# Kernel optimization log

Measured on AMD Instinct MI355X. Metric: run time of the kernel, lower is better.

Reference implementation:

```python
import jax, jax.numpy as jnp
import numpy as np

N, E = 100000, 1000000
IN_F, HID, OUT, K = 64, 64, 32, 3


def setup_inputs() -> dict:
    key = jax.random.key(0)
    ks = jax.random.split(key, 8)
    s = 0.05
    return {
        "features": jax.random.normal(ks[0], (N, IN_F), dtype=jnp.float32),
        "src": jax.random.randint(ks[1], (E,), 0, N),
        "dst": jax.random.randint(ks[2], (E,), 0, N),
        "n_nodes": N,
        "W1": jax.random.normal(ks[3], (K * IN_F, HID), jnp.float32) * s,
        "b1": jnp.zeros((HID,), jnp.float32),
        "W2": jax.random.normal(ks[4], (K * HID, HID), jnp.float32) * s,
        "b2": jnp.zeros((HID,), jnp.float32),
        "Wm1": jax.random.normal(ks[5], (HID, HID), jnp.float32) * s,
        "bm1": jnp.zeros((HID,), jnp.float32),
        "Wm2": jax.random.normal(ks[6], (HID, OUT), jnp.float32) * s,
        "bm2": jnp.zeros((OUT,), jnp.float32),
    }


def _cheb_conv(x, src, dst, dinv, W, b, n_nodes, k=K):
    # DGL ChebConv with lambda_max = 2 (re_norm = 2/lambda_max = 1).
    def prop(h):  # D^{-1/2} A D^{-1/2} h via edge gather/scatter
        m = (h * dinv)[src]                                   # [E, F]
        agg = jax.ops.segment_sum(m, dst, num_segments=n_nodes)
        return agg * dinv

    X0 = x
    Xs = [X0]
    X1 = -prop(X0)                 # -re_norm*L h + (re_norm-1)*X0, re_norm=1
    Xs.append(X1)
    for _ in range(2, k):
        Xi = -2.0 * prop(X1) - X0  # Chebyshev recursion
        Xs.append(Xi)
        X0, X1 = X1, Xi
    return jnp.concatenate(Xs, axis=1) @ W + b  # Linear(k*F_in -> F_out)


def reference(features, src, dst, n_nodes, W1, b1, W2, b2, Wm1, bm1, Wm2, bm2):
    deg = jax.ops.segment_sum(
        jnp.ones((src.shape[0],), dtype=features.dtype), dst, num_segments=n_nodes
    )
    dinv = (jnp.clip(deg, 1.0, None) ** -0.5)[:, None]  # in-degree^{-1/2}
    x = jax.nn.relu(_cheb_conv(features, src, dst, dinv, W1, b1, n_nodes))
    x = jax.nn.relu(_cheb_conv(x, src, dst, dinv, W2, b2, n_nodes))
    return jax.nn.relu(x @ Wm1 + bm1) @ Wm2 + bm2
```

## Files before the change

### kernel.cpp

```cpp
#include <hip/hip_runtime.h>


typedef unsigned short ushort_t;

__device__ inline ushort_t f2bf(float f) {
    unsigned u = __float_as_uint(f);
    return (ushort_t)((u + 0x7FFFu + ((u >> 16) & 1u)) >> 16);
}
__device__ inline float bf2f(ushort_t h) {
    return __uint_as_float(((unsigned)h) << 16);
}

#define BSH 9
#define BSZ (1 << BSH)
#define CHUNK 4096

__global__ __launch_bounds__(256) void k_bhist(const int* __restrict__ dst,
                                               int* __restrict__ gbase, int E, int NB) {
    __shared__ int h[1024];
    for (int i = threadIdx.x; i < NB; i += 256) h[i] = 0;
    __syncthreads();
    for (int i = blockIdx.x * blockDim.x + threadIdx.x; i < E; i += gridDim.x * blockDim.x)
        atomicAdd(&h[dst[i] >> BSH], 1);
    __syncthreads();
    for (int i = threadIdx.x; i < NB; i += 256)
        if (h[i]) atomicAdd(&gbase[i], h[i]);
}

__global__ void k_bscan(int* __restrict__ gbase, int* __restrict__ gcur, int NB) {
    __shared__ int sh[1024];
    int t = threadIdx.x;
    int v = (t < NB) ? gbase[t] : 0;
    sh[t] = v;
    __syncthreads();
    for (int off = 1; off < 1024; off <<= 1) {
        int u = 0;
        if (t >= off) u = sh[t - off];
        __syncthreads();
        sh[t] += u;
        __syncthreads();
    }
    if (t < NB) {
        int excl = sh[t] - v;
        gbase[t] = excl;
        gcur[t] = excl;
    }
}

__global__ __launch_bounds__(256) void k_bucket2(
    const int* __restrict__ src, const int* __restrict__ dst,
    int* __restrict__ gcur, int2* __restrict__ eb, int E, int NB) {
    __shared__ int ls[CHUNK];
    __shared__ int ld[CHUNK];
    __shared__ int hist[1024];
    __shared__ int bbase[1024];
    int t = threadIdx.x;
    int base = blockIdx.x * CHUNK;
    int count = E - base;
    if (count > CHUNK) count = CHUNK;
    for (int i = t; i < NB; i += 256) hist[i] = 0;
    __syncthreads();
    for (int i = t; i < count; i += 256) {
        int s = src[base + i];
        int d = dst[base + i];
        ls[i] = s;
        ld[i] = d;
        atomicAdd(&hist[d >> BSH], 1);
    }
    __syncthreads();
    for (int b = t; b < NB; b += 256) {
        int c = hist[b];
        bbase[b] = c ? atomicAdd(&gcur[b], c) : 0;
        hist[b] = 0;
    }
    __syncthreads();
    for (int i = t; i < count; i += 256) {
        int d = ld[i];
        int b = d >> BSH;
        int off = atomicAdd(&hist[b], 1);
        eb[bbase[b] + off] = make_int2(ls[i], d);
    }
}

__global__ __launch_bounds__(256) void k_local(
    const int2* __restrict__ eb, const int* __restrict__ gbase,
    int* __restrict__ col, int* __restrict__ row_ptr,
    float* __restrict__ dinv, int N, int E, int NB) {
    __shared__ int cnt[BSZ];
    __shared__ int tsum[256];
    int t = threadIdx.x;
    int b = blockIdx.x;
    int d0 = b << BSH;
    cnt[2 * t] = 0;
    cnt[2 * t + 1] = 0;
    __syncthreads();
    int beg = gbase[b];
    int end = (b + 1 < NB) ? gbase[b + 1] : E;
    for (int i = beg + t; i < end; i += 256)
        atomicAdd(&cnt[eb[i].y - d0], 1);
    __syncthreads();
    int c0 = cnt[2 * t], c1 = cnt[2 * t + 1];
    int mysum = c0 + c1;
    tsum[t] = mysum;
    __syncthreads();
    for (int off = 1; off < 256; off <<= 1) {
        int u = 0;
        if (t >= off) u = tsum[t - off];
        __syncthreads();
        tsum[t] += u;
        __syncthreads();
    }
    int rbase = beg + tsum[t] - mysum;
    int d = d0 + 2 * t;
    if (d < N) {
        row_ptr[d] = rbase;
        dinv[d] = rsqrtf(fmaxf((float)c0, 1.0f));
    }
    if (d + 1 < N) {
        row_ptr[d + 1] = rbase + c0;
        dinv[d + 1] = rsqrtf(fmaxf((float)c1, 1.0f));
    }
    cnt[2 * t] = rbase;
    cnt[2 * t + 1] = rbase + c0;
    __syncthreads();
    for (int i = beg + t; i < end; i += 256) {
        int2 e = eb[i];
        int p = atomicAdd(&cnt[e.y - d0], 1);
        col[p] = e.x;
    }
    if (b == NB - 1 && t == 0) row_ptr[N] = E;
}

__global__ void k_tobf16(const float4* __restrict__ X, const float* __restrict__ dinv,
                         ushort4* __restrict__ Y, int n4) {
    int i = blockIdx.x * blockDim.x + threadIdx.x;
    if (i < n4) {
        float s = dinv[i >> 4];
        float4 v = X[i];
        ushort4 o;
        o.x = f2bf(v.x * s); o.y = f2bf(v.y * s); o.z = f2bf(v.z * s); o.w = f2bf(v.w * s);
        Y[i] = o;
    }
}

template <int MODE>
__global__ __launch_bounds__(256) void k_prop(
    const ushort_t* __restrict__ Xb, const int* __restrict__ rp,
    const int* __restrict__ col, const float* __restrict__ dinv,
    const ushort_t* __restrict__ X0b, ushort_t* __restrict__ OUTB, int N) {
    int wid = (blockIdx.x * blockDim.x + threadIdx.x) >> 6;
    int lane = threadIdx.x & 63;
    if (wid >= N) return;
    int g = lane >> 4;
    int fl = (lane & 15) * 4;
    int beg = rp[wid], end = rp[wid + 1];
    float4 a0 = make_float4(0.f, 0.f, 0.f, 0.f);
    float4 a1 = make_float4(0.f, 0.f, 0.f, 0.f);
    int e = beg + g;
    for (; e + 4 < end; e += 8) {
        int s0 = col[e], s1 = col[e + 4];
        ushort4 u0 = *(const ushort4*)&Xb[(size_t)s0 * 64 + fl];
        ushort4 u1 = *(const ushort4*)&Xb[(size_t)s1 * 64 + fl];
        a0.x += bf2f(u0.x); a0.y += bf2f(u0.y); a0.z += bf2f(u0.z); a0.w += bf2f(u0.w);
        a1.x += bf2f(u1.x); a1.y += bf2f(u1.y); a1.z += bf2f(u1.z); a1.w += bf2f(u1.w);
    }
    if (e < end) {
        int s0 = col[e];
        ushort4 u0 = *(const ushort4*)&Xb[(size_t)s0 * 64 + fl];
        a0.x += bf2f(u0.x); a0.y += bf2f(u0.y); a0.z += bf2f(u0.z); a0.w += bf2f(u0.w);
    }
    float4 acc;
    acc.x = a0.x + a1.x;
    acc.y = a0.y + a1.y;
    acc.z = a0.z + a1.z;
    acc.w = a0.w + a1.w;
    acc.x += __shfl_xor(acc.x, 16);
    acc.y += __shfl_xor(acc.y, 16);
    acc.z += __shfl_xor(acc.z, 16);
    acc.w += __shfl_xor(acc.w, 16);
    acc.x += __shfl_xor(acc.x, 32);
    acc.y += __shfl_xor(acc.y, 32);
    acc.z += __shfl_xor(acc.z, 32);
    acc.w += __shfl_xor(acc.w, 32);
    if (g == 0) {
        float di = dinv[wid];
        float4 o;
        if (MODE == 1) {
            float m = -di * di;
            o.x = m * acc.x; o.y = m * acc.y; o.z = m * acc.z; o.w = m * acc.w;
        } else {
            ushort4 x0u = *(const ushort4*)&X0b[(size_t)wid * 64 + fl];
            float m = -2.0f * di;
            float rd = 1.0f / di;
            o.x = fmaf(m, acc.x, -rd * bf2f(x0u.x));
            o.y = fmaf(m, acc.y, -rd * bf2f(x0u.y));
            o.z = fmaf(m, acc.z, -rd * bf2f(x0u.z));
            o.w = fmaf(m, acc.w, -rd * bf2f(x0u.w));
        }
        ushort4 ob;
        ob.x = f2bf(o.x); ob.y = f2bf(o.y); ob.z = f2bf(o.z); ob.w = f2bf(o.w);
        *(ushort4*)&OUTB[(size_t)wid * 64 + fl] = ob;
    }
}

template <bool SCALE_OUT>
__global__ __launch_bounds__(256) void k_cheb_gemm(
    const ushort_t* __restrict__ X0, const ushort_t* __restrict__ X1,
    const ushort_t* __restrict__ X2, const float* __restrict__ dinv,
    const float* __restrict__ W, const float* __restrict__ b,
    ushort_t* __restrict__ Yb, int N) {
    __shared__ float Ws[64][64];
    __shared__ float Xs[64][68];
    __shared__ float bs[64];
    int t = threadIdx.x;
    if (t < 64) bs[t] = b[t];

    int c4 = (t & 15) * 4;
    int r4 = (t >> 4) * 4;
    int node0 = blockIdx.x * 64;
    float acc[4][4] = {{0}};

    const ushort_t* Xp[3] = {X0, X1, X2};
#pragma unroll 1
    for (int chunk = 0; chunk < 3; chunk++) {
        __syncthreads();
        {
            const float* Wc = W + chunk * 64 * 64;
            for (int i = t; i < 64 * 16; i += 256) {
                int r = i >> 4, c = (i & 15) * 4;
                *(float4*)&Ws[r][c] = *(const float4*)&Wc[r * 64 + c];
            }
        }
        {
            const ushort_t* X = Xp[chunk];
            bool unscale = (chunk < 2);
            int f4 = (t & 15) * 4;
            int nl0 = t >> 4;
            for (int p = 0; p < 4; p++) {
                int nl = nl0 + p * 16;
                int node = node0 + nl;
                float4 v = make_float4(0.f, 0.f, 0.f, 0.f);
                if (node < N) {
                    ushort4 u = *(const ushort4*)&X[(size_t)node * 64 + f4];
                    float r = unscale ? (1.0f / dinv[node]) : 1.0f;
                    v = make_float4(r * bf2f(u.x), r * bf2f(u.y),
                                    r * bf2f(u.z), r * bf2f(u.w));
                }
                *(float4*)&Xs[nl][f4] = v;
            }
        }
        __syncthreads();
#pragma unroll 4
        for (int k4 = 0; k4 < 64; k4 += 4) {
            float4 xv[4], wv[4];
#pragma unroll
            for (int i = 0; i < 4; i++) xv[i] = *(const float4*)&Xs[r4 + i][k4];
#pragma unroll
            for (int q = 0; q < 4; q++) wv[q] = *(const float4*)&Ws[k4 + q][c4];
#pragma unroll
            for (int i = 0; i < 4; i++) {
                acc[i][0] = fmaf(xv[i].x, wv[0].x, acc[i][0]);
                acc[i][1] = fmaf(xv[i].x, wv[0].y, acc[i][1]);
                acc[i][2] = fmaf(xv[i].x, wv[0].z, acc[i][2]);
                acc[i][3] = fmaf(xv[i].x, wv[0].w, acc[i][3]);
                acc[i][0] = fmaf(xv[i].y, wv[1].x, acc[i][0]);
                acc[i][1] = fmaf(xv[i].y, wv[1].y, acc[i][1]);
                acc[i][2] = fmaf(xv[i].y, wv[1].z, acc[i][2]);
                acc[i][3] = fmaf(xv[i].y, wv[1].w, acc[i][3]);
                acc[i][0] = fmaf(xv[i].z, wv[2].x, acc[i][0]);
                acc[i][1] = fmaf(xv[i].z, wv[2].y, acc[i][1]);
                acc[i][2] = fmaf(xv[i].z, wv[2].z, acc[i][2]);
                acc[i][3] = fmaf(xv[i].z, wv[2].w, acc[i][3]);
                acc[i][0] = fmaf(xv[i].w, wv[3].x, acc[i][0]);
                acc[i][1] = fmaf(xv[i].w, wv[3].y, acc[i][1]);
                acc[i][2] = fmaf(xv[i].w, wv[3].z, acc[i][2]);
                acc[i][3] = fmaf(xv[i].w, wv[3].w, acc[i][3]);
            }
        }
    }
#pragma unroll
    for (int i = 0; i < 4; i++) {
        int row = node0 + r4 + i;
        if (row < N) {
            float s = SCALE_OUT ? dinv[row] : 1.0f;
            ushort4 ob;
            ob.x = f2bf(s * fmaxf(acc[i][0] + bs[c4 + 0], 0.0f));
            ob.y = f2bf(s * fmaxf(acc[i][1] + bs[c4 + 1], 0.0f));
            ob.z = f2bf(s * fmaxf(acc[i][2] + bs[c4 + 2], 0.0f));
            ob.w = f2bf(s * fmaxf(acc[i][3] + bs[c4 + 3], 0.0f));
            *(ushort4*)&Yb[(size_t)row * 64 + c4] = ob;
        }
    }
}

__global__ __launch_bounds__(256) void k_mlp_gemm(
    const ushort_t* __restrict__ Hb, const float* __restrict__ Wm1,
    const float* __restrict__ bm1, const float* __restrict__ Wm2,
    const float* __restrict__ bm2, float* __restrict__ out, int N) {
    __shared__ float W1s[64][64];
    __shared__ float W2s[64][32];
    __shared__ float Hs[64][68];
    __shared__ float b1s[64];
    __shared__ float b2s[32];
    int t = threadIdx.x;
    for (int i = t; i < 64 * 16; i += 256) {
        int r = i >> 4, c = (i & 15) * 4;
        *(float4*)&W1s[r][c] = *(const float4*)&Wm1[r * 64 + c];
    }
    for (int i = t; i < 64 * 8; i += 256) {
        int r = i >> 3, c = (i & 7) * 4;
        *(float4*)&W2s[r][c] = *(const float4*)&Wm2[r * 32 + c];
    }
    if (t < 64) b1s[t] = bm1[t];
    else if (t < 96) b2s[t - 64] = bm2[t - 64];

    int node0 = blockIdx.x * 64;
    {
        int f4 = (t & 15) * 4;
        int nl0 = t >> 4;
        for (int p = 0; p < 4; p++) {
            int nl = nl0 + p * 16;
            int node = node0 + nl;
            float4 v = make_float4(0.f, 0.f, 0.f, 0.f);
            if (node < N) {
                ushort4 u = *(const ushort4*)&Hb[(size_t)node * 64 + f4];
                v = make_float4(bf2f(u.x), bf2f(u.y), bf2f(u.z), bf2f(u.w));
            }
            *(float4*)&Hs[nl][f4] = v;
        }
    }
    __syncthreads();

    float acc[4][4] = {{0}};
    int c4 = (t & 15) * 4;
    int r4 = (t >> 4) * 4;
#pragma unroll 4
    for (int k4 = 0; k4 < 64; k4 += 4) {
        float4 xv[4], wv[4];
#pragma unroll
        for (int i = 0; i < 4; i++) xv[i] = *(const float4*)&Hs[r4 + i][k4];
#pragma unroll
        for (int q = 0; q < 4; q++) wv[q] = *(const float4*)&W1s[k4 + q][c4];
#pragma unroll
        for (int i = 0; i < 4; i++) {
            acc[i][0] = fmaf(xv[i].x, wv[0].x, acc[i][0]);
            acc[i][1] = fmaf(xv[i].x, wv[0].y, acc[i][1]);
            acc[i][2] = fmaf(xv[i].x, wv[0].z, acc[i][2]);
            acc[i][3] = fmaf(xv[i].x, wv[0].w, acc[i][3]);
            acc[i][0] = fmaf(xv[i].y, wv[1].x, acc[i][0]);
            acc[i][1] = fmaf(xv[i].y, wv[1].y, acc[i][1]);
            acc[i][2] = fmaf(xv[i].y, wv[1].z, acc[i][2]);
            acc[i][3] = fmaf(xv[i].y, wv[1].w, acc[i][3]);
            acc[i][0] = fmaf(xv[i].z, wv[2].x, acc[i][0]);
            acc[i][1] = fmaf(xv[i].z, wv[2].y, acc[i][1]);
            acc[i][2] = fmaf(xv[i].z, wv[2].z, acc[i][2]);
            acc[i][3] = fmaf(xv[i].z, wv[2].w, acc[i][3]);
            acc[i][0] = fmaf(xv[i].w, wv[3].x, acc[i][0]);
            acc[i][1] = fmaf(xv[i].w, wv[3].y, acc[i][1]);
            acc[i][2] = fmaf(xv[i].w, wv[3].z, acc[i][2]);
            acc[i][3] = fmaf(xv[i].w, wv[3].w, acc[i][3]);
        }
    }
    __syncthreads();
#pragma unroll
    for (int i = 0; i < 4; i++) {
        float4 o;
        o.x = fmaxf(acc[i][0] + b1s[c4 + 0], 0.0f);
        o.y = fmaxf(acc[i][1] + b1s[c4 + 1], 0.0f);
        o.z = fmaxf(acc[i][2] + b1s[c4 + 2], 0.0f);
        o.w = fmaxf(acc[i][3] + b1s[c4 + 3], 0.0f);
        *(float4*)&Hs[r4 + i][c4] = o;
    }
    __syncthreads();

    {
        int cc4 = (t & 7) * 4;
        int r2 = (t >> 3) * 2;
        float a2[2][4] = {{0}};
#pragma unroll 4
        for (int k4 = 0; k4 < 64; k4 += 4) {
            float4 xv[2], wv[4];
#pragma unroll
            for (int i = 0; i < 2; i++) xv[i] = *(const float4*)&Hs[r2 + i][k4];
#pragma unroll
            for (int q = 0; q < 4; q++) wv[q] = *(const float4*)&W2s[k4 + q][cc4];
#pragma unroll
            for (int i = 0; i < 2; i++) {
                a2[i][0] = fmaf(xv[i].x, wv[0].x, a2[i][0]);
                a2[i][1] = fmaf(xv[i].x, wv[0].y, a2[i][1]);
                a2[i][2] = fmaf(xv[i].x, wv[0].z, a2[i][2]);
                a2[i][3] = fmaf(xv[i].x, wv[0].w, a2[i][3]);
                a2[i][0] = fmaf(xv[i].y, wv[1].x, a2[i][0]);
                a2[i][1] = fmaf(xv[i].y, wv[1].y, a2[i][1]);
                a2[i][2] = fmaf(xv[i].y, wv[1].z, a2[i][2]);
                a2[i][3] = fmaf(xv[i].y, wv[1].w, a2[i][3]);
                a2[i][0] = fmaf(xv[i].z, wv[2].x, a2[i][0]);
                a2[i][1] = fmaf(xv[i].z, wv[2].y, a2[i][1]);
                a2[i][2] = fmaf(xv[i].z, wv[2].z, a2[i][2]);
                a2[i][3] = fmaf(xv[i].z, wv[2].w, a2[i][3]);
                a2[i][0] = fmaf(xv[i].w, wv[3].x, a2[i][0]);
                a2[i][1] = fmaf(xv[i].w, wv[3].y, a2[i][1]);
                a2[i][2] = fmaf(xv[i].w, wv[3].z, a2[i][2]);
                a2[i][3] = fmaf(xv[i].w, wv[3].w, a2[i][3]);
            }
        }
#pragma unroll
        for (int i = 0; i < 2; i++) {
            int row = node0 + r2 + i;
            if (row < N) {
                float4 o;
                o.x = a2[i][0] + b2s[cc4 + 0];
                o.y = a2[i][1] + b2s[cc4 + 1];
                o.z = a2[i][2] + b2s[cc4 + 2];
                o.w = a2[i][3] + b2s[cc4 + 3];
                *(float4*)&out[(size_t)row * 32 + cc4] = o;
            }
        }
    }
}

extern "C" void kernel_launch(void* const* d_in, const int* in_sizes, int n_in,
                              void* d_out, int out_size, void* d_ws, size_t ws_size,
                              hipStream_t stream) {
    const float* features = (const float*)d_in[0];
    const int* src = (const int*)d_in[1];
    const int* dst = (const int*)d_in[2];
    const float* W1 = (const float*)d_in[4];
    const float* b1 = (const float*)d_in[5];
    const float* W2 = (const float*)d_in[6];
    const float* b2 = (const float*)d_in[7];
    const float* Wm1 = (const float*)d_in[8];
    const float* bm1 = (const float*)d_in[9];
    const float* Wm2 = (const float*)d_in[10];
    const float* bm2 = (const float*)d_in[11];
    float* out = (float*)d_out;

    int N = in_sizes[0] / 64;
    int E = in_sizes[1];
    int NB = (N + BSZ - 1) >> BSH;

    float* ws = (float*)d_ws;
    float* dinv = ws;
    int* row_ptr = (int*)(dinv + N);
    int* gbase = row_ptr + (N + 1);
    int* gcur = gbase + 1024;
    int* col = gcur + 1024;
    int2* eb = (int2*)(((uintptr_t)(col + E) + 7) & ~(uintptr_t)7);
    ushort_t* Fb  = (ushort_t*)(eb + E);
    ushort_t* X1b = Fb  + (size_t)N * 64;
    ushort_t* X2b = X1b + (size_t)N * 64;
    ushort_t* H1b = X2b + (size_t)N * 64;
    ushort_t* H2b = H1b + (size_t)N * 64;

    int pblk = (N * 64 + 255) / 256;
    int gblk = (N + 63) / 64;
    int n4 = N * 16;
    int cblk = (n4 + 255) / 256;
    int bblk = (E + CHUNK - 1) / CHUNK;

    hipMemsetAsync(gbase, 0, NB * sizeof(int), stream);
    k_bhist<<<512, 256, 0, stream>>>(dst, gbase, E, NB);
    k_bscan<<<1, 1024, 0, stream>>>(gbase, gcur, NB);
    k_bucket2<<<bblk, 256, 0, stream>>>(src, dst, gcur, eb, E, NB);
    k_local<<<NB, 256, 0, stream>>>(eb, gbase, col, row_ptr, dinv, N, E, NB);

    k_tobf16<<<cblk, 256, 0, stream>>>((const float4*)features, dinv, (ushort4*)Fb, n4);

    k_prop<1><<<pblk, 256, 0, stream>>>(Fb, row_ptr, col, dinv, nullptr, X1b, N);
    k_prop<2><<<pblk, 256, 0, stream>>>(X1b, row_ptr, col, dinv, Fb, X2b, N);
    k_cheb_gemm<true><<<gblk, 256, 0, stream>>>(Fb, X1b, X2b, dinv, W1, b1, H1b, N);

    k_prop<1><<<pblk, 256, 0, stream>>>(H1b, row_ptr, col, dinv, nullptr, X1b, N);
    k_prop<2><<<pblk, 256, 0, stream>>>(X1b, row_ptr, col, dinv, H1b, X2b, N);
    k_cheb_gemm<false><<<gblk, 256, 0, stream>>>(H1b, X1b, X2b, dinv, W2, b2, H2b, N);

    k_mlp_gemm<<<gblk, 256, 0, stream>>>(H2b, Wm1, bm1, Wm2, bm2, out, N);
}
```

Baseline: 429.1 us.

## Replace FP32 SIMT GEMMs with bf16 MFMA for Chebyshev and MLP layers

Rewrites the Chebyshev linear layers and the final MLP to use 16x16x32 bf16 MFMA instructions. A new prep kernel converts the weights to transposed bf16. The Chebyshev GEMM keeps separate accumulators for the dinv-scaled and unscaled chunks, so the per-row rescale moves from the operand load into the epilogue. This removes the shared-memory staging and FP32 FMA loops, but quantises the weights to bf16 and writes outputs with narrower, scalar stores.

```diff
diff --git a/kernel.cpp b/kernel.cpp
--- a/kernel.cpp
+++ b/kernel.cpp
@@ -2,6 +2,8 @@
 
 
 typedef unsigned short ushort_t;
+typedef __attribute__((ext_vector_type(8))) short v8s;
+typedef __attribute__((ext_vector_type(4))) float v4f;
 
 __device__ inline ushort_t f2bf(float f) {
     unsigned u = __float_as_uint(f);
@@ -14,6 +16,7 @@
 #define BSH 9
 #define BSZ (1 << BSH)
 #define CHUNK 4096
+
 
 __global__ __launch_bounds__(256) void k_bhist(const int* __restrict__ dst,
                                                int* __restrict__ gbase, int E, int NB) {
@@ -129,6 +132,20 @@
         col[p] = e.x;
     }
     if (b == NB - 1 && t == 0) row_ptr[N] = E;
+}
+
+__global__ void k_wprep(const float* __restrict__ W1, const float* __restrict__ W2,
+                        const float* __restrict__ Wm1, const float* __restrict__ Wm2,
+                        ushort_t* __restrict__ W1t, ushort_t* __restrict__ W2t,
+                        ushort_t* __restrict__ Wm1t, ushort_t* __restrict__ Wm2t) {
+    int i = blockIdx.x * 256 + threadIdx.x;
+    if (i < 12288) { int k = i >> 6, n = i & 63; W1t[n * 192 + k] = f2bf(W1[i]); return; }
+    i -= 12288;
+    if (i < 12288) { int k = i >> 6, n = i & 63; W2t[n * 192 + k] = f2bf(W2[i]); return; }
+    i -= 12288;
+    if (i < 4096) { int k = i >> 6, n = i & 63; Wm1t[n * 64 + k] = f2bf(Wm1[i]); return; }
+    i -= 4096;
+    if (i < 2048) { int k = i >> 5, n = i & 31; Wm2t[n * 64 + k] = f2bf(Wm2[i]); }
 }
 
 __global__ void k_tobf16(const float4* __restrict__ X, const float* __restrict__ dinv,
@@ -204,217 +221,111 @@
 }
 
 template <bool SCALE_OUT>
-__global__ __launch_bounds__(256) void k_cheb_gemm(
+__global__ __launch_bounds__(256) void k_cheb_mfma(
     const ushort_t* __restrict__ X0, const ushort_t* __restrict__ X1,
     const ushort_t* __restrict__ X2, const float* __restrict__ dinv,
-    const float* __restrict__ W, const float* __restrict__ b,
-    ushort_t* __restrict__ Yb, int N) {
-    __shared__ float Ws[64][64];
-    __shared__ float Xs[64][68];
-    __shared__ float bs[64];
-    int t = threadIdx.x;
-    if (t < 64) bs[t] = b[t];
-
-    int c4 = (t & 15) * 4;
-    int r4 = (t >> 4) * 4;
+    const ushort_t* __restrict__ Wt,
+    const float* __restrict__ b, ushort_t* __restrict__ Yb, int N) {
+    int wave = threadIdx.x >> 6, lane = threadIdx.x & 63;
+    int n16 = lane & 15, q = lane >> 4;
     int node0 = blockIdx.x * 64;
-    float acc[4][4] = {{0}};
-
-    const ushort_t* Xp[3] = {X0, X1, X2};
-#pragma unroll 1
-    for (int chunk = 0; chunk < 3; chunk++) {
-        __syncthreads();
-        {
-            const float* Wc = W + chunk * 64 * 64;
-            for (int i = t; i < 64 * 16; i += 256) {
-                int r = i >> 4, c = (i & 15) * 4;
-                *(float4*)&Ws[r][c] = *(const float4*)&Wc[r * 64 + c];
+    int arow = node0 + wave * 16 + n16;
+    const ushort_t* Xc[3] = {X0, X1, X2};
+
+    v4f acc_s[4], acc_u[4];
+#pragma unroll
+    for (int t = 0; t < 4; t++) {
+        acc_s[t] = (v4f){0.f, 0.f, 0.f, 0.f};
+        acc_u[t] = (v4f){0.f, 0.f, 0.f, 0.f};
+    }
+
+#pragma unroll
+    for (int ks = 0; ks < 6; ks++) {
+        int c = ks >> 1;
+        int kk = (ks & 1) * 32 + q * 8;
+        v8s av = {0, 0, 0, 0, 0, 0, 0, 0};
+        if (arow < N) av = *(const v8s*)&Xc[c][(size_t)arow * 64 + kk];
+#pragma unroll
+        for (int t = 0; t < 4; t++) {
+            v8s bv = *(const v8s*)&Wt[(size_t)(t * 16 + n16) * 192 + ks * 32 + q * 8];
+            if (c < 2)
+                acc_s[t] = __builtin_amdgcn_mfma_f32_16x16x32_bf16(av, bv, acc_s[t], 0, 0, 0);
+            else
+                acc_u[t] = __builtin_amdgcn_mfma_f32_16x16x32_bf16(av, bv, acc_u[t], 0, 0, 0);
+        }
+    }
+
+    int rbase = node0 + wave * 16 + q * 4;
+#pragma unroll
+    for (int r = 0; r < 4; r++) {
+        int row = rbase + r;
+        if (row < N) {
+            float dv = dinv[row];
+            float rd = 1.0f / dv;
+            float s = SCALE_OUT ? dv : 1.0f;
+#pragma unroll
+            for (int t = 0; t < 4; t++) {
+                float y = fmaf(rd, acc_s[t][r], acc_u[t][r]) + b[t * 16 + n16];
+                y = fmaxf(y, 0.0f);
+                Yb[(size_t)row * 64 + t * 16 + n16] = f2bf(s * y);
             }
         }
-        {
-            const ushort_t* X = Xp[chunk];
-            bool unscale = (chunk < 2);
-            int f4 = (t & 15) * 4;
-            int nl0 = t >> 4;
-            for (int p = 0; p < 4; p++) {
-                int nl = nl0 + p * 16;
-                int node = node0 + nl;
-                float4 v = make_float4(0.f, 0.f, 0.f, 0.f);
-                if (node < N) {
-                    ushort4 u = *(const ushort4*)&X[(size_t)node * 64 + f4];
-                    float r = unscale ? (1.0f / dinv[node]) : 1.0f;
-                    v = make_float4(r * bf2f(u.x), r * bf2f(u.y),
-                                    r * bf2f(u.z), r * bf2f(u.w));
-                }
-                *(float4*)&Xs[nl][f4] = v;
-            }
-        }
-        __syncthreads();
-#pragma unroll 4
-        for (int k4 = 0; k4 < 64; k4 += 4) {
-            float4 xv[4], wv[4];
-#pragma unroll
-            for (int i = 0; i < 4; i++) xv[i] = *(const float4*)&Xs[r4 + i][k4];
-#pragma unroll
-            for (int q = 0; q < 4; q++) wv[q] = *(const float4*)&Ws[k4 + q][c4];
-#pragma unroll
-            for (int i = 0; i < 4; i++) {
-                acc[i][0] = fmaf(xv[i].x, wv[0].x, acc[i][0]);
-                acc[i][1] = fmaf(xv[i].x, wv[0].y, acc[i][1]);
-                acc[i][2] = fmaf(xv[i].x, wv[0].z, acc[i][2]);
-                acc[i][3] = fmaf(xv[i].x, wv[0].w, acc[i][3]);
-                acc[i][0] = fmaf(xv[i].y, wv[1].x, acc[i][0]);
-                acc[i][1] = fmaf(xv[i].y, wv[1].y, acc[i][1]);
-                acc[i][2] = fmaf(xv[i].y, wv[1].z, acc[i][2]);
-                acc[i][3] = fmaf(xv[i].y, wv[1].w, acc[i][3]);
-                acc[i][0] = fmaf(xv[i].z, wv[2].x, acc[i][0]);
-                acc[i][1] = fmaf(xv[i].z, wv[2].y, acc[i][1]);
-                acc[i][2] = fmaf(xv[i].z, wv[2].z, acc[i][2]);
-                acc[i][3] = fmaf(xv[i].z, wv[2].w, acc[i][3]);
-                acc[i][0] = fmaf(xv[i].w, wv[3].x, acc[i][0]);
-                acc[i][1] = fmaf(xv[i].w, wv[3].y, acc[i][1]);
-                acc[i][2] = fmaf(xv[i].w, wv[3].z, acc[i][2]);
-                acc[i][3] = fmaf(xv[i].w, wv[3].w, acc[i][3]);
-            }
-        }
-    }
-#pragma unroll
-    for (int i = 0; i < 4; i++) {
-        int row = node0 + r4 + i;
+    }
+}
+
+__global__ __launch_bounds__(256) void k_mlp_mfma(
+    const ushort_t* __restrict__ Hb, const ushort_t* __restrict__ W1t,
+    const float* __restrict__ b1, const ushort_t* __restrict__ W2t,
+    const float* __restrict__ b2, float* __restrict__ out, int N) {
+    __shared__ ushort_t Hs[64][76];
+    int wave = threadIdx.x >> 6, lane = threadIdx.x & 63;
+    int n16 = lane & 15, q = lane >> 4;
+    int node0 = blockIdx.x * 64;
+    int arow = node0 + wave * 16 + n16;
+
+    v4f acc[4];
+#pragma unroll
+    for (int t = 0; t < 4; t++) acc[t] = (v4f){0.f, 0.f, 0.f, 0.f};
+#pragma unroll
+    for (int ks = 0; ks < 2; ks++) {
+        v8s av = {0, 0, 0, 0, 0, 0, 0, 0};
+        if (arow < N) av = *(const v8s*)&Hb[(size_t)arow * 64 + ks * 32 + q * 8];
+#pragma unroll
+        for (int t = 0; t < 4; t++) {
+            v8s bv = *(const v8s*)&W1t[(size_t)(t * 16 + n16) * 64 + ks * 32 + q * 8];
+            acc[t] = __builtin_amdgcn_mfma_f32_16x16x32_bf16(av, bv, acc[t], 0, 0, 0);
+        }
+    }
+    int lr = wave * 16 + q * 4;
+#pragma unroll
+    for (int r = 0; r < 4; r++)
+#pragma unroll
+        for (int t = 0; t < 4; t++) {
+            float y = acc[t][r] + b1[t * 16 + n16];
+            Hs[lr + r][t * 16 + n16] = f2bf(fmaxf(y, 0.0f));
+        }
+    __syncthreads();
+
+    v4f a2[2];
+    a2[0] = (v4f){0.f, 0.f, 0.f, 0.f};
+    a2[1] = (v4f){0.f, 0.f, 0.f, 0.f};
+#pragma unroll
+    for (int ks = 0; ks < 2; ks++) {
+        v8s av = *(const v8s*)&Hs[wave * 16 + n16][ks * 32 + q * 8];
+#pragma unroll
+        for (int t = 0; t < 2; t++) {
+            v8s bv = *(const v8s*)&W2t[(size_t)(t * 16 + n16) * 64 + ks * 32 + q * 8];
+            a2[t] = __builtin_amdgcn_mfma_f32_16x16x32_bf16(av, bv, a2[t], 0, 0, 0);
+        }
+    }
+    int rbase = node0 + wave * 16 + q * 4;
+#pragma unroll
+    for (int r = 0; r < 4; r++) {
+        int row = rbase + r;
         if (row < N) {
-            float s = SCALE_OUT ? dinv[row] : 1.0f;
-            ushort4 ob;
-            ob.x = f2bf(s * fmaxf(acc[i][0] + bs[c4 + 0], 0.0f));
-            ob.y = f2bf(s * fmaxf(acc[i][1] + bs[c4 + 1], 0.0f));
-            ob.z = f2bf(s * fmaxf(acc[i][2] + bs[c4 + 2], 0.0f));
-            ob.w = f2bf(s * fmaxf(acc[i][3] + bs[c4 + 3], 0.0f));
-            *(ushort4*)&Yb[(size_t)row * 64 + c4] = ob;
-        }
-    }
-}
-
-__global__ __launch_bounds__(256) void k_mlp_gemm(
-    const ushort_t* __restrict__ Hb, const float* __restrict__ Wm1,
-    const float* __restrict__ bm1, const float* __restrict__ Wm2,
-    const float* __restrict__ bm2, float* __restrict__ out, int N) {
-    __shared__ float W1s[64][64];
-    __shared__ float W2s[64][32];
-    __shared__ float Hs[64][68];
-    __shared__ float b1s[64];
-    __shared__ float b2s[32];
-    int t = threadIdx.x;
-    for (int i = t; i < 64 * 16; i += 256) {
-        int r = i >> 4, c = (i & 15) * 4;
-        *(float4*)&W1s[r][c] = *(const float4*)&Wm1[r * 64 + c];
-    }
-    for (int i = t; i < 64 * 8; i += 256) {
-        int r = i >> 3, c = (i & 7) * 4;
-        *(float4*)&W2s[r][c] = *(const float4*)&Wm2[r * 32 + c];
-    }
-    if (t < 64) b1s[t] = bm1[t];
-    else if (t < 96) b2s[t - 64] = bm2[t - 64];
-
-    int node0 = blockIdx.x * 64;
-    {
-        int f4 = (t & 15) * 4;
-        int nl0 = t >> 4;
-        for (int p = 0; p < 4; p++) {
-            int nl = nl0 + p * 16;
-            int node = node0 + nl;
-            float4 v = make_float4(0.f, 0.f, 0.f, 0.f);
-            if (node < N) {
-                ushort4 u = *(const ushort4*)&Hb[(size_t)node * 64 + f4];
-                v = make_float4(bf2f(u.x), bf2f(u.y), bf2f(u.z), bf2f(u.w));
-            }
-            *(float4*)&Hs[nl][f4] = v;
-        }
-    }
-    __syncthreads();
-
-    float acc[4][4] = {{0}};
-    int c4 = (t & 15) * 4;
-    int r4 = (t >> 4) * 4;
-#pragma unroll 4
-    for (int k4 = 0; k4 < 64; k4 += 4) {
-        float4 xv[4], wv[4];
-#pragma unroll
-        for (int i = 0; i < 4; i++) xv[i] = *(const float4*)&Hs[r4 + i][k4];
-#pragma unroll
-        for (int q = 0; q < 4; q++) wv[q] = *(const float4*)&W1s[k4 + q][c4];
-#pragma unroll
-        for (int i = 0; i < 4; i++) {
-            acc[i][0] = fmaf(xv[i].x, wv[0].x, acc[i][0]);
-            acc[i][1] = fmaf(xv[i].x, wv[0].y, acc[i][1]);
-            acc[i][2] = fmaf(xv[i].x, wv[0].z, acc[i][2]);
-            acc[i][3] = fmaf(xv[i].x, wv[0].w, acc[i][3]);
-            acc[i][0] = fmaf(xv[i].y, wv[1].x, acc[i][0]);
-            acc[i][1] = fmaf(xv[i].y, wv[1].y, acc[i][1]);
-            acc[i][2] = fmaf(xv[i].y, wv[1].z, acc[i][2]);
-            acc[i][3] = fmaf(xv[i].y, wv[1].w, acc[i][3]);
-            acc[i][0] = fmaf(xv[i].z, wv[2].x, acc[i][0]);
-            acc[i][1] = fmaf(xv[i].z, wv[2].y, acc[i][1]);
-            acc[i][2] = fmaf(xv[i].z, wv[2].z, acc[i][2]);
-            acc[i][3] = fmaf(xv[i].z, wv[2].w, acc[i][3]);
-            acc[i][0] = fmaf(xv[i].w, wv[3].x, acc[i][0]);
-            acc[i][1] = fmaf(xv[i].w, wv[3].y, acc[i][1]);
-            acc[i][2] = fmaf(xv[i].w, wv[3].z, acc[i][2]);
-            acc[i][3] = fmaf(xv[i].w, wv[3].w, acc[i][3]);
-        }
-    }
-    __syncthreads();
-#pragma unroll
-    for (int i = 0; i < 4; i++) {
-        float4 o;
-        o.x = fmaxf(acc[i][0] + b1s[c4 + 0], 0.0f);
-        o.y = fmaxf(acc[i][1] + b1s[c4 + 1], 0.0f);
-        o.z = fmaxf(acc[i][2] + b1s[c4 + 2], 0.0f);
-        o.w = fmaxf(acc[i][3] + b1s[c4 + 3], 0.0f);
-        *(float4*)&Hs[r4 + i][c4] = o;
-    }
-    __syncthreads();
-
-    {
-        int cc4 = (t & 7) * 4;
-        int r2 = (t >> 3) * 2;
-        float a2[2][4] = {{0}};
-#pragma unroll 4
-        for (int k4 = 0; k4 < 64; k4 += 4) {
-            float4 xv[2], wv[4];
-#pragma unroll
-            for (int i = 0; i < 2; i++) xv[i] = *(const float4*)&Hs[r2 + i][k4];
-#pragma unroll
-            for (int q = 0; q < 4; q++) wv[q] = *(const float4*)&W2s[k4 + q][cc4];
-#pragma unroll
-            for (int i = 0; i < 2; i++) {
-                a2[i][0] = fmaf(xv[i].x, wv[0].x, a2[i][0]);
-                a2[i][1] = fmaf(xv[i].x, wv[0].y, a2[i][1]);
-                a2[i][2] = fmaf(xv[i].x, wv[0].z, a2[i][2]);
-                a2[i][3] = fmaf(xv[i].x, wv[0].w, a2[i][3]);
-                a2[i][0] = fmaf(xv[i].y, wv[1].x, a2[i][0]);
-                a2[i][1] = fmaf(xv[i].y, wv[1].y, a2[i][1]);
-                a2[i][2] = fmaf(xv[i].y, wv[1].z, a2[i][2]);
-                a2[i][3] = fmaf(xv[i].y, wv[1].w, a2[i][3]);
-                a2[i][0] = fmaf(xv[i].z, wv[2].x, a2[i][0]);
-                a2[i][1] = fmaf(xv[i].z, wv[2].y, a2[i][1]);
-                a2[i][2] = fmaf(xv[i].z, wv[2].z, a2[i][2]);
-                a2[i][3] = fmaf(xv[i].z, wv[2].w, a2[i][3]);
-                a2[i][0] = fmaf(xv[i].w, wv[3].x, a2[i][0]);
-                a2[i][1] = fmaf(xv[i].w, wv[3].y, a2[i][1]);
-                a2[i][2] = fmaf(xv[i].w, wv[3].z, a2[i][2]);
-                a2[i][3] = fmaf(xv[i].w, wv[3].w, a2[i][3]);
-            }
-        }
-#pragma unroll
-        for (int i = 0; i < 2; i++) {
-            int row = node0 + r2 + i;
-            if (row < N) {
-                float4 o;
-                o.x = a2[i][0] + b2s[cc4 + 0];
-                o.y = a2[i][1] + b2s[cc4 + 1];
-                o.z = a2[i][2] + b2s[cc4 + 2];
-                o.w = a2[i][3] + b2s[cc4 + 3];
-                *(float4*)&out[(size_t)row * 32 + cc4] = o;
-            }
+#pragma unroll
+            for (int t = 0; t < 2; t++)
+                out[(size_t)row * 32 + t * 16 + n16] = a2[t][r] + b2[t * 16 + n16];
         }
     }
 }
@@ -451,6 +362,10 @@
     ushort_t* X2b = X1b + (size_t)N * 64;
     ushort_t* H1b = X2b + (size_t)N * 64;
     ushort_t* H2b = H1b + (size_t)N * 64;
+    ushort_t* W1t = H2b + (size_t)N * 64;
+    ushort_t* W2t = W1t + 64 * 192;
+    ushort_t* Wm1t = W2t + 64 * 192;
+    ushort_t* Wm2t = Wm1t + 64 * 64;
 
     int pblk = (N * 64 + 255) / 256;
     int gblk = (N + 63) / 64;
@@ -458,6 +373,8 @@
     int cblk = (n4 + 255) / 256;
     int bblk = (E + CHUNK - 1) / CHUNK;
 
+    k_wprep<<<(30720 + 255) / 256, 256, 0, stream>>>(W1, W2, Wm1, Wm2, W1t, W2t, Wm1t, Wm2t);
+
     hipMemsetAsync(gbase, 0, NB * sizeof(int), stream);
     k_bhist<<<512, 256, 0, stream>>>(dst, gbase, E, NB);
     k_bscan<<<1, 1024, 0, stream>>>(gbase, gcur, NB);
@@ -468,11 +385,11 @@
 
     k_prop<1><<<pblk, 256, 0, stream>>>(Fb, row_ptr, col, dinv, nullptr, X1b, N);
     k_prop<2><<<pblk, 256, 0, stream>>>(X1b, row_ptr, col, dinv, Fb, X2b, N);
-    k_cheb_gemm<true><<<gblk, 256, 0, stream>>>(Fb, X1b, X2b, dinv, W1, b1, H1b, N);
+    k_cheb_mfma<true><<<gblk, 256, 0, stream>>>(Fb, X1b, X2b, dinv, W1t, b1, H1b, N);
 
     k_prop<1><<<pblk, 256, 0, stream>>>(H1b, row_ptr, col, dinv, nullptr, X1b, N);
     k_prop<2><<<pblk, 256, 0, stream>>>(X1b, row_ptr, col, dinv, H1b, X2b, N);
-    k_cheb_gemm<false><<<gblk, 256, 0, stream>>>(H1b, X1b, X2b, dinv, W2, b2, H2b, N);
-
-    k_mlp_gemm<<<gblk, 256, 0, stream>>>(H2b, Wm1, bm1, Wm2, bm2, out, N);
-}
+    k_cheb_mfma<false><<<gblk, 256, 0, stream>>>(H1b, X1b, X2b, dinv, W2t, b2, H2b, N);
+
+    k_mlp_mfma<<<gblk, 256, 0, stream>>>(H2b, Wm1t, bm1, Wm2t, bm2, out, N);
+}
```

Result: faster. 395.9 us (-7.7%).
